# Kernel tuning notes

Measured on AMD Instinct MI355X. Metric: run time of the kernel, lower is better.

## Reference

```python
import jax, jax.numpy as jnp
import numpy as np

B, L, H, D = 64, 256, 16, 64   # batch, seq_len, heads, head_dim
C, K = 256, 8                  # wavelet c (== seq_len, required by attn@V), k
FACTOR = 5
SAMPLE_K = min(FACTOR * int(np.ceil(np.log(L))), C)  # U_part = 30
N_TOP = min(FACTOR * int(np.ceil(np.log(L))), C)     # u = 30
SCALE = 1.0 / float(np.sqrt(D))
ICH = L * D                    # Linear in-features: flattened (seq_len*D)
CK = C * K


def setup_inputs() -> dict:
    key = jax.random.key(0)
    ks = jax.random.split(key, 10)
    std = 1.0 / float(np.sqrt(ICH))
    def lin(kw, kb):
        return (jax.random.uniform(kw, (CK, ICH), jnp.float32, -std, std),
                jax.random.uniform(kb, (CK,), jnp.float32, -std, std))
    Wq_w, Wq_b = lin(ks[3], ks[4])
    Wk_w, Wk_b = lin(ks[5], ks[6])
    Wv_w, Wv_b = lin(ks[7], ks[8])
    return {
        "queries": jax.random.normal(ks[0], (B, L, H, D), jnp.float32),
        "keys":    jax.random.normal(ks[1], (B, L, H, D), jnp.float32),
        "values":  jax.random.normal(ks[2], (B, L, H, D), jnp.float32),
        "Wq_w": Wq_w, "Wq_b": Wq_b,
        "Wk_w": Wk_w, "Wk_b": Wk_b,
        "Wv_w": Wv_w, "Wv_b": Wv_b,
        "index_sample": jax.random.randint(ks[9], (C, SAMPLE_K), 0, C),
        "attn_mask": jnp.zeros((1,), bool),  # unused: module overwrites it with ProbMask
    }


def reference(queries, keys, values, Wq_w, Wq_b, Wk_w, Wk_b, Wv_w, Wv_b, index_sample, attn_mask):
    # [B,L,H,D] -> [B,H,L,D]
    q = jnp.swapaxes(queries, 1, 2)
    k = jnp.swapaxes(keys, 1, 2)
    v = jnp.swapaxes(values, 1, 2)

    def wavelet(x, W, b):
        # flatten (L,D) per head, project to c*k, reshape to [B,H,C,K]
        return (x.reshape(B, H, L * D) @ W.T + b).reshape(B, H, C, K)

    qw = wavelet(q, Wq_w, Wq_b)   # [B,H,C,K]
    kw = wavelet(k, Wk_w, Wk_b)   # [B,H,C,K]
    _vw = wavelet(v, Wv_w, Wv_b)  # computed then unused, as in the torch source

    # _prob_QK: sample SAMPLE_K keys per query position
    K_samp = kw[:, :, index_sample, :]                        # [B,H,C,S,K]
    QKs = jnp.einsum('bhck,bhcsk->bhcs', qw, K_samp)          # [B,H,C,S]
    M = QKs.max(-1) - QKs.sum(-1) / C                         # sparsity measure
    idx = jax.lax.top_k(M, N_TOP)[1]                          # [B,H,U] top queries
    Q_red = jnp.take_along_axis(qw, idx[..., None], axis=2)   # [B,H,U,K]
    scores = jnp.einsum('bhuk,bhck->bhuc', Q_red, kw) * SCALE # [B,H,U,C]

    # ProbMask: causal triu(1) rows gathered at idx
    tri = jnp.triu(jnp.ones((L, C), bool), 1)
    scores = jnp.where(tri[idx], -jnp.inf, scores)
    attn = jax.nn.softmax(scores, axis=-1)

    # initial context = cumsum of V (mask_flag=True); scatter updated rows
    ctx = jnp.cumsum(v, axis=2)                               # [B,H,L,D]
    upd = jnp.einsum('bhuc,bhcd->bhud', attn, v)              # C == L
    b_i = jnp.arange(B)[:, None, None]
    h_i = jnp.arange(H)[None, :, None]
    return ctx.at[b_i, h_i, idx].set(upd)                     # [B,H,L,D]
```

## Files before the change

### kernel.cpp

```cpp
#include <hip/hip_runtime.h>

#define NC 256
#define NK 8
#define NS 30
#define ICHN 16384
#define CKN 2048
#define MROWS 1024
#define PLANE ((size_t)MROWS * CKN)
#define SCLQ (1.0f / 65536.0f)

typedef _Float16 h4 __attribute__((ext_vector_type(4)));
typedef _Float16 h8 __attribute__((ext_vector_type(8)));
typedef float f4v __attribute__((ext_vector_type(4)));

__device__ __forceinline__ void split4(const float4& x, h4& hi, h4& lo) {
  const float* xp = &x.x;
#pragma unroll
  for (int j = 0; j < 4; ++j) {
    float xs = xp[j] * 256.0f;
    _Float16 hh = (_Float16)xs;
    hi[j] = hh;
    lo[j] = (_Float16)(xs - (float)hh);
  }
}

__global__ __launch_bounds__(512, 2) void gemm_split3(
    const float* __restrict__ qin, const float* __restrict__ kin,
    const float* __restrict__ Wq, const float* __restrict__ Wk,
    float* __restrict__ P, int KS, int KL, int nsteps) {
  __shared__ __align__(16) _Float16 ldsA[2][256][64];
  __shared__ __align__(16) _Float16 ldsB[2][256][64];

  const int tm = blockIdx.x & 3;
  const int tn = blockIdx.x >> 2;
  const int ksi = blockIdx.y;
  const int z = blockIdx.z;
  const float* act = z ? kin : qin;
  const float* W = z ? Wk : Wq;
  float* outp = P + (size_t)(z * KS + ksi) * PLANE;

  const int tid = threadIdx.x;
  const int r = tid >> 1;
  const int g = tid & 1;
  const int R = tm * 256 + r;
  const float* aP = act + (size_t)(R >> 4) * 262144 + (R & 15) * 64 +
                    (size_t)ksi * KL * 16 + g * 16;
  const int n = tn * 256 + r;
  const float* bP = W + (size_t)n * 16384 + (size_t)ksi * KL + g * 16;

  const int swW = r & 7;
  const int oh0 = r * 64 + (((4 * g + 0) ^ swW) << 3);
  const int ol0 = r * 64 + (((4 * g + 1) ^ swW) << 3);
  const int oh1 = r * 64 + (((4 * g + 2) ^ swW) << 3);
  const int ol1 = r * 64 + (((4 * g + 3) ^ swW) << 3);

  const int lane = tid & 63;
  const int wv = tid >> 6;
  const int wm = wv >> 2;
  const int wn = wv & 3;
  const int lr = lane & 15;
  const int lk = lane >> 4;
  const int swR = lr & 7;
  const int aOffH = (wm * 128 + lr) * 64 + (((2 * lk) ^ swR) << 3);
  const int aOffL = (wm * 128 + lr) * 64 + (((2 * lk + 1) ^ swR) << 3);
  const int bOffH = (wn * 64 + lr) * 64 + (((2 * lk) ^ swR) << 3);
  const int bOffL = (wn * 64 + lr) * 64 + (((2 * lk + 1) ^ swR) << 3);

  f4v acc[8][4];
#pragma unroll
  for (int i = 0; i < 8; ++i)
#pragma unroll
    for (int j = 0; j < 4; ++j) acc[i][j] = (f4v){0.f, 0.f, 0.f, 0.f};

  float4 aS[4], bS[4];

  auto LOADT = [&](int s) {
    const size_t aoff = (size_t)(s >> 1) * 1024 + (s & 1) * 32;
    const size_t boff = (size_t)s * 32;
#pragma unroll
    for (int c = 0; c < 4; ++c) {
      aS[c] = *(const float4*)(aP + aoff + c * 4);
      bS[c] = *(const float4*)(bP + boff + c * 4);
    }
  };
  auto WRITES = [&](int bufi) {
    _Float16* bA = &ldsA[bufi][0][0];
    _Float16* bB = &ldsB[bufi][0][0];
    h4 h0, l0, h1, l1;
    split4(aS[0], h0, l0);
    split4(aS[1], h1, l1);
    *(h8*)(bA + oh0) = (h8){h0[0], h0[1], h0[2], h0[3], h1[0], h1[1], h1[2], h1[3]};
    *(h8*)(bA + ol0) = (h8){l0[0], l0[1], l0[2], l0[3], l1[0], l1[1], l1[2], l1[3]};
    split4(aS[2], h0, l0);
    split4(aS[3], h1, l1);
    *(h8*)(bA + oh1) = (h8){h0[0], h0[1], h0[2], h0[3], h1[0], h1[1], h1[2], h1[3]};
    *(h8*)(bA + ol1) = (h8){l0[0], l0[1], l0[2], l0[3], l1[0], l1[1], l1[2], l1[3]};
    split4(bS[0], h0, l0);
    split4(bS[1], h1, l1);
    *(h8*)(bB + oh0) = (h8){h0[0], h0[1], h0[2], h0[3], h1[0], h1[1], h1[2], h1[3]};
    *(h8*)(bB + ol0) = (h8){l0[0], l0[1], l0[2], l0[3], l1[0], l1[1], l1[2], l1[3]};
    split4(bS[2], h0, l0);
    split4(bS[3], h1, l1);
    *(h8*)(bB + oh1) = (h8){h0[0], h0[1], h0[2], h0[3], h1[0], h1[1], h1[2], h1[3]};
    *(h8*)(bB + ol1) = (h8){l0[0], l0[1], l0[2], l0[3], l1[0], l1[1], l1[2], l1[3]};
  };
  auto COMPUTE = [&](int bufi) {
    const _Float16* bA = &ldsA[bufi][0][0];
    const _Float16* bB = &ldsB[bufi][0][0];
    h8 Bh[4], Bl[4];
#pragma unroll
    for (int fn = 0; fn < 4; ++fn) {
      Bh[fn] = *(const h8*)(bB + bOffH + fn * 1024);
      Bl[fn] = *(const h8*)(bB + bOffL + fn * 1024);
    }
#pragma unroll
    for (int half = 0; half < 2; ++half) {
      h8 Ah[4], Al[4];
#pragma unroll
      for (int fr = 0; fr < 4; ++fr) {
        Ah[fr] = *(const h8*)(bA + aOffH + (half * 4 + fr) * 1024);
        Al[fr] = *(const h8*)(bA + aOffL + (half * 4 + fr) * 1024);
      }
      __builtin_amdgcn_s_setprio(1);
#pragma unroll
      for (int fr = 0; fr < 4; ++fr)
#pragma unroll
        for (int fn = 0; fn < 4; ++fn) {
          f4v a = acc[half * 4 + fr][fn];
          a = __builtin_amdgcn_mfma_f32_16x16x32_f16(Ah[fr], Bh[fn], a, 0, 0, 0);
          a = __builtin_amdgcn_mfma_f32_16x16x32_f16(Ah[fr], Bl[fn], a, 0, 0, 0);
          a = __builtin_amdgcn_mfma_f32_16x16x32_f16(Al[fr], Bh[fn], a, 0, 0, 0);
          acc[half * 4 + fr][fn] = a;
        }
      __builtin_amdgcn_s_setprio(0);
    }
  };

  LOADT(0);
  WRITES(0);
  __syncthreads();
  int cur = 0;
  for (int s = 0; s < nsteps; ++s) {
    if (s + 1 < nsteps) LOADT(s + 1);
    COMPUTE(cur);
    if (s + 1 < nsteps) WRITES(cur ^ 1);
    __syncthreads();
    cur ^= 1;
  }

#pragma unroll
  for (int fr = 0; fr < 8; ++fr)
#pragma unroll
    for (int fn = 0; fn < 4; ++fn) {
      int ocol = tn * 256 + wn * 64 + fn * 16 + lr;
#pragma unroll
      for (int j = 0; j < 4; ++j) {
        int orow = tm * 256 + wm * 128 + fr * 16 + lk * 4 + j;
        outp[(size_t)orow * CKN + ocol] = acc[fr][fn][j];
      }
    }
}

__global__ __launch_bounds__(256, 2) void attn_tail(
    const float* __restrict__ P, const float* __restrict__ bq,
    const float* __restrict__ bk, const float* __restrict__ values,
    const int* __restrict__ isamp, float* __restrict__ out, int KS) {
  __shared__ float kT[8][256];
  __shared__ __align__(16) _Float16 vT[64][256];
  __shared__ __align__(16) _Float16 Pm[32][256];
  __shared__ float qsel[NS][8];
  __shared__ float MvC[256];
  __shared__ float csum4[4][64];
  __shared__ int idxl[NS];
  __shared__ int flagl[256];

  const int bh = blockIdx.x;
  const int b = bh >> 4, h = bh & 15;
  const int tid = threadIdx.x;
  const int w = tid >> 6, lane = tid & 63;
  const float* qpl = P;
  const float* kpl = P + (size_t)KS * PLANE;
  float* obase = out + (size_t)bh * 16384;

  float qq[8];
  {
    float ks8[8];
    size_t rowo = (size_t)bh * CKN + tid * 8;
#pragma unroll
    for (int k = 0; k < 8; ++k) ks8[k] = 0.0f;
    for (int p = 0; p < KS; ++p) {
      float4 a0 = *(const float4*)(kpl + p * PLANE + rowo);
      float4 a1 = *(const float4*)(kpl + p * PLANE + rowo + 4);
      ks8[0] += a0.x; ks8[1] += a0.y; ks8[2] += a0.z; ks8[3] += a0.w;
      ks8[4] += a1.x; ks8[5] += a1.y; ks8[6] += a1.z; ks8[7] += a1.w;
    }
    float4 b0 = *(const float4*)(bk + tid * 8);
    float4 b1 = *(const float4*)(bk + tid * 8 + 4);
    const float* bp = &b0.x;
    kT[0][tid] = ks8[0] * SCLQ + b0.x; kT[1][tid] = ks8[1] * SCLQ + b0.y;
    kT[2][tid] = ks8[2] * SCLQ + b0.z; kT[3][tid] = ks8[3] * SCLQ + b0.w;
    kT[4][tid] = ks8[4] * SCLQ + b1.x; kT[5][tid] = ks8[5] * SCLQ + b1.y;
    kT[6][tid] = ks8[6] * SCLQ + b1.z; kT[7][tid] = ks8[7] * SCLQ + b1.w;
    (void)bp;
#pragma unroll
    for (int k = 0; k < 8; ++k) qq[k] = 0.0f;
    for (int p = 0; p < KS; ++p) {
      float4 a0 = *(const float4*)(qpl + p * PLANE + rowo);
      float4 a1 = *(const float4*)(qpl + p * PLANE + rowo + 4);
      qq[0] += a0.x; qq[1] += a0.y; qq[2] += a0.z; qq[3] += a0.w;
      qq[4] += a1.x; qq[5] += a1.y; qq[6] += a1.z; qq[7] += a1.w;
    }
    float4 c0 = *(const float4*)(bq + tid * 8);
    float4 c1 = *(const float4*)(bq + tid * 8 + 4);
    qq[0] = qq[0] * SCLQ + c0.x; qq[1] = qq[1] * SCLQ + c0.y;
    qq[2] = qq[2] * SCLQ + c0.z; qq[3] = qq[3] * SCLQ + c0.w;
    qq[4] = qq[4] * SCLQ + c1.x; qq[5] = qq[5] * SCLQ + c1.y;
    qq[6] = qq[6] * SCLQ + c1.z; qq[7] = qq[7] * SCLQ + c1.w;
    const float* vbase = values + (size_t)b * 262144 + h * 64;
#pragma unroll
    for (int rep = 0; rep < 16; ++rep) {
      int i = rep * 256 + tid;
      int c = i >> 4, dg = i & 15;
      float4 v = *(const float4*)(vbase + (size_t)c * 1024 + dg * 4);
      const float* vp = &v.x;
#pragma unroll
      for (int j = 0; j < 4; ++j) {
        int d = dg * 4 + j;
        vT[d][(((c >> 3) ^ (d & 7)) << 3) | (c & 7)] = (_Float16)vp[j];
      }
    }
    flagl[tid] = 0;
    if (tid < 64) {
#pragma unroll
      for (int rr = 30; rr < 32; ++rr) {
        int ci = tid >> 1;
        *(h4*)&Pm[rr][((ci ^ (rr & 7)) << 3) | ((tid * 4) & 7)] =
            (h4){(_Float16)0, (_Float16)0, (_Float16)0, (_Float16)0};
      }
    }
  }
  __syncthreads();

  {
    float mx = -INFINITY, sm = 0.0f;
    const int* ip = isamp + tid * NS;
#pragma unroll 6
    for (int s = 0; s < NS; ++s) {
      int j = ip[s];
      float dot = 0.0f;
#pragma unroll
      for (int k = 0; k < NK; ++k) dot += qq[k] * kT[k][j];
      mx = fmaxf(mx, dot);
      sm += dot;
    }
    MvC[tid] = mx - sm * (1.0f / 256.0f);
  }
  __syncthreads();

  if (tid < 64) {
    float m0 = MvC[tid], m1 = MvC[tid + 64], m2 = MvC[tid + 128], m3 = MvC[tid + 192];
    for (int u = 0; u < NS; ++u) {
      float bv = m0; int bi = tid;
      if (m1 > bv) { bv = m1; bi = tid + 64; }
      if (m2 > bv) { bv = m2; bi = tid + 128; }
      if (m3 > bv) { bv = m3; bi = tid + 192; }
#pragma unroll
      for (int off = 32; off > 0; off >>= 1) {
        float ov = __shfl_xor(bv, off);
        int oi = __shfl_xor(bi, off);
        if (ov > bv || (ov == bv && oi < bi)) { bv = ov; bi = oi; }
      }
      if (tid == 0) { idxl[u] = bi; flagl[bi] = u + 1; }
      if (tid == (bi & 63)) {
        switch (bi >> 6) {
          case 0: m0 = -INFINITY; break;
          case 1: m1 = -INFINITY; break;
          case 2: m2 = -INFINITY; break;
          default: m3 = -INFINITY; break;
        }
      }
    }
  }
  __syncthreads();

  if (tid < NS * 8) {
    int u = tid >> 3, k = tid & 7;
    size_t off = (size_t)bh * CKN + idxl[u] * 8 + k;
    float s = 0.0f;
    for (int p = 0; p < KS; ++p) s += qpl[p * PLANE + off];
    qsel[u][k] = s * SCLQ + bq[idxl[u] * 8 + k];
  }
  __syncthreads();

  for (int ui = w; ui < NS; ui += 4) {
    const int qi = idxl[ui];
    float qv[8];
#pragma unroll
    for (int k = 0; k < 8; ++k) qv[k] = qsel[ui][k];
    float sj[4];
#pragma unroll
    for (int j = 0; j < 4; ++j) {
      int c = j * 64 + lane;
      float s = 0.0f;
#pragma unroll
      for (int k = 0; k < NK; ++k) s += qv[k] * kT[k][c];
      sj[j] = (c > qi) ? -INFINITY : s * 0.125f;
    }
    float m = fmaxf(fmaxf(sj[0], sj[1]), fmaxf(sj[2], sj[3]));
#pragma unroll
    for (int off = 32; off > 0; off >>= 1) m = fmaxf(m, __shfl_xor(m, off));
    float pj[4], ts = 0.0f;
#pragma unroll
    for (int j = 0; j < 4; ++j) { pj[j] = __expf(sj[j] - m); ts += pj[j]; }
#pragma unroll
    for (int off = 32; off > 0; off >>= 1) ts += __shfl_xor(ts, off);
    float rinv = 1.0f / ts;
#pragma unroll
    for (int j = 0; j < 4; ++j) {
      int c = j * 64 + lane;
      Pm[ui][(((c >> 3) ^ (ui & 7)) << 3) | (c & 7)] = (_Float16)(pj[j] * rinv);
    }
  }
  __syncthreads();

  {
    const int lr = lane & 15, lk = lane >> 4;
    f4v pacc[2];
    pacc[0] = (f4v){0.f, 0.f, 0.f, 0.f};
    pacc[1] = (f4v){0.f, 0.f, 0.f, 0.f};
#pragma unroll
    for (int kc = 0; kc < 8; ++kc) {
      int cidx = kc * 4 + lk;
      h8 Bv = *(const h8*)&vT[w * 16 + lr][((cidx ^ (lr & 7)) << 3)];
#pragma unroll
      for (int mf = 0; mf < 2; ++mf) {
        h8 Ap = *(const h8*)&Pm[mf * 16 + lr][((cidx ^ (lr & 7)) << 3)];
        pacc[mf] = __builtin_amdgcn_mfma_f32_16x16x32_f16(Ap, Bv, pacc[mf], 0, 0, 0);
      }
    }
#pragma unroll
    for (int mf = 0; mf < 2; ++mf)
#pragma unroll
      for (int j = 0; j < 4; ++j) {
        int u = mf * 16 + lk * 4 + j;
        if (u < NS) obase[(size_t)idxl[u] * 64 + w * 16 + lr] = pacc[mf][j];
      }
  }

  {
    float cs = 0.0f;
#pragma unroll 8
    for (int i = 0; i < 64; ++i) {
      int c = w * 64 + i;
      cs += (float)vT[lane][(((c >> 3) ^ (lane & 7)) << 3) | (c & 7)];
    }
    csum4[w][lane] = cs;
    __syncthreads();
    float run = 0.0f;
    for (int j2 = 0; j2 < w; ++j2) run += csum4[j2][lane];
    for (int i = 0; i < 64; ++i) {
      int l = w * 64 + i;
      run += (float)vT[lane][(((l >> 3) ^ (lane & 7)) << 3) | (l & 7)];
      if (!flagl[l]) obase[(size_t)l * 64 + lane] = run;
    }
  }
}

extern "C" void kernel_launch(void* const* d_in, const int* in_sizes, int n_in,
                              void* d_out, int out_size, void* d_ws, size_t ws_size,
                              hipStream_t stream) {
  (void)in_sizes; (void)n_in; (void)out_size;
  const float* queries = (const float*)d_in[0];
  const float* keys = (const float*)d_in[1];
  const float* values = (const float*)d_in[2];
  const float* Wq_w = (const float*)d_in[3];
  const float* Wq_b = (const float*)d_in[4];
  const float* Wk_w = (const float*)d_in[5];
  const float* Wk_b = (const float*)d_in[6];
  const int* index_sample = (const int*)d_in[9];
  float* out = (float*)d_out;

  float* P = (float*)d_ws;

  const int KS = (ws_size >= (size_t)8 * PLANE * 4) ? 4 : 2;
  const int KL = ICHN / KS;
  const int nsteps = KL / 32;

  dim3 gridG(32, KS, 2);
  gemm_split3<<<gridG, 512, 0, stream>>>(queries, keys, Wq_w, Wk_w, P, KS, KL, nsteps);
  attn_tail<<<dim3(MROWS), 256, 0, stream>>>(P, Wq_b, Wk_b, values, index_sample, out, KS);
}
```

Baseline: 454.9 us.

## Interleave global prefetch, LDS reads and split MFMA phases; remap block order

The GEMM main loop is split into three MFMA phases, with fragment reads from shared memory and the global prefetch loads for A and B spread between them and separated by extra barriers, so memory latency hides behind matrix instructions. The grid becomes 1D with the row tile as the slowest index, so blocks that share the same activation rows run at nearby times and reuse the activation data in cache. This adds two more block-wide barriers per k-step and keeps more fragments live in registers at once, which could lower occupancy or cause spills.

```diff
diff --git a/kernel.cpp b/kernel.cpp
--- a/kernel.cpp
+++ b/kernel.cpp
@@ -27,32 +27,34 @@
 __global__ __launch_bounds__(512, 2) void gemm_split3(
     const float* __restrict__ qin, const float* __restrict__ kin,
     const float* __restrict__ Wq, const float* __restrict__ Wk,
-    float* __restrict__ P, int KS, int KL, int nsteps) {
+    float* __restrict__ P, int KS, int KL, int nsteps, int groups) {
   __shared__ __align__(16) _Float16 ldsA[2][256][64];
   __shared__ __align__(16) _Float16 ldsB[2][256][64];
 
-  const int tm = blockIdx.x & 3;
-  const int tn = blockIdx.x >> 2;
-  const int ksi = blockIdx.y;
-  const int z = blockIdx.z;
+  const int bx = blockIdx.x;
+  const int tm = bx / groups;
+  const int g = bx - tm * groups;
+  const int tn = g & 7;
+  const int ksi = (g >> 3) % KS;
+  const int z = g / (8 * KS);
   const float* act = z ? kin : qin;
   const float* W = z ? Wk : Wq;
   float* outp = P + (size_t)(z * KS + ksi) * PLANE;
 
   const int tid = threadIdx.x;
   const int r = tid >> 1;
-  const int g = tid & 1;
+  const int gg = tid & 1;
   const int R = tm * 256 + r;
   const float* aP = act + (size_t)(R >> 4) * 262144 + (R & 15) * 64 +
-                    (size_t)ksi * KL * 16 + g * 16;
+                    (size_t)ksi * KL * 16 + gg * 16;
   const int n = tn * 256 + r;
-  const float* bP = W + (size_t)n * 16384 + (size_t)ksi * KL + g * 16;
+  const float* bP = W + (size_t)n * 16384 + (size_t)ksi * KL + gg * 16;
 
   const int swW = r & 7;
-  const int oh0 = r * 64 + (((4 * g + 0) ^ swW) << 3);
-  const int ol0 = r * 64 + (((4 * g + 1) ^ swW) << 3);
-  const int oh1 = r * 64 + (((4 * g + 2) ^ swW) << 3);
-  const int ol1 = r * 64 + (((4 * g + 3) ^ swW) << 3);
+  const int oh0 = r * 64 + (((4 * gg + 0) ^ swW) << 3);
+  const int ol0 = r * 64 + (((4 * gg + 1) ^ swW) << 3);
+  const int oh1 = r * 64 + (((4 * gg + 2) ^ swW) << 3);
+  const int ol1 = r * 64 + (((4 * gg + 3) ^ swW) << 3);
 
   const int lane = tid & 63;
   const int wv = tid >> 6;
@@ -73,15 +75,17 @@
     for (int j = 0; j < 4; ++j) acc[i][j] = (f4v){0.f, 0.f, 0.f, 0.f};
 
   float4 aS[4], bS[4];
-
-  auto LOADT = [&](int s) {
+  h8 Bh[4], Bl[4], A0h[4], A0l[4], A1h[4], A1l[4];
+
+  auto LOADT_A = [&](int s) {
     const size_t aoff = (size_t)(s >> 1) * 1024 + (s & 1) * 32;
+#pragma unroll
+    for (int c = 0; c < 4; ++c) aS[c] = *(const float4*)(aP + aoff + c * 4);
+  };
+  auto LOADT_B = [&](int s) {
     const size_t boff = (size_t)s * 32;
 #pragma unroll
-    for (int c = 0; c < 4; ++c) {
-      aS[c] = *(const float4*)(aP + aoff + c * 4);
-      bS[c] = *(const float4*)(bP + boff + c * 4);
-    }
+    for (int c = 0; c < 4; ++c) bS[c] = *(const float4*)(bP + boff + c * 4);
   };
   auto WRITES = [&](int bufi) {
     _Float16* bA = &ldsA[bufi][0][0];
@@ -104,46 +108,87 @@
     *(h8*)(bB + oh1) = (h8){h0[0], h0[1], h0[2], h0[3], h1[0], h1[1], h1[2], h1[3]};
     *(h8*)(bB + ol1) = (h8){l0[0], l0[1], l0[2], l0[3], l1[0], l1[1], l1[2], l1[3]};
   };
-  auto COMPUTE = [&](int bufi) {
-    const _Float16* bA = &ldsA[bufi][0][0];
-    const _Float16* bB = &ldsB[bufi][0][0];
-    h8 Bh[4], Bl[4];
+
+  auto READ_B = [&](int bufi) {
+    const _Float16* b = &ldsB[bufi][0][0];
 #pragma unroll
     for (int fn = 0; fn < 4; ++fn) {
-      Bh[fn] = *(const h8*)(bB + bOffH + fn * 1024);
-      Bl[fn] = *(const h8*)(bB + bOffL + fn * 1024);
-    }
-#pragma unroll
-    for (int half = 0; half < 2; ++half) {
-      h8 Ah[4], Al[4];
-#pragma unroll
-      for (int fr = 0; fr < 4; ++fr) {
-        Ah[fr] = *(const h8*)(bA + aOffH + (half * 4 + fr) * 1024);
-        Al[fr] = *(const h8*)(bA + aOffL + (half * 4 + fr) * 1024);
-      }
-      __builtin_amdgcn_s_setprio(1);
-#pragma unroll
-      for (int fr = 0; fr < 4; ++fr)
-#pragma unroll
-        for (int fn = 0; fn < 4; ++fn) {
-          f4v a = acc[half * 4 + fr][fn];
-          a = __builtin_amdgcn_mfma_f32_16x16x32_f16(Ah[fr], Bh[fn], a, 0, 0, 0);
-          a = __builtin_amdgcn_mfma_f32_16x16x32_f16(Ah[fr], Bl[fn], a, 0, 0, 0);
-          a = __builtin_amdgcn_mfma_f32_16x16x32_f16(Al[fr], Bh[fn], a, 0, 0, 0);
-          acc[half * 4 + fr][fn] = a;
-        }
-      __builtin_amdgcn_s_setprio(0);
-    }
-  };
-
-  LOADT(0);
+      Bh[fn] = *(const h8*)(b + bOffH + fn * 1024);
+      Bl[fn] = *(const h8*)(b + bOffL + fn * 1024);
+    }
+  };
+  auto READ_A0 = [&](int bufi) {
+    const _Float16* a = &ldsA[bufi][0][0];
+#pragma unroll
+    for (int fr = 0; fr < 4; ++fr) {
+      A0h[fr] = *(const h8*)(a + aOffH + fr * 1024);
+      A0l[fr] = *(const h8*)(a + aOffL + fr * 1024);
+    }
+  };
+  auto READ_A1 = [&](int bufi) {
+    const _Float16* a = &ldsA[bufi][0][0];
+#pragma unroll
+    for (int fr = 0; fr < 4; ++fr) {
+      A1h[fr] = *(const h8*)(a + aOffH + (4 + fr) * 1024);
+      A1l[fr] = *(const h8*)(a + aOffL + (4 + fr) * 1024);
+    }
+  };
+  auto MFMA_A = [&]() {
+    __builtin_amdgcn_s_setprio(1);
+#pragma unroll
+    for (int fr = 0; fr < 4; ++fr)
+#pragma unroll
+      for (int fn = 0; fn < 4; ++fn) {
+        f4v a = acc[fr][fn];
+        a = __builtin_amdgcn_mfma_f32_16x16x32_f16(A0h[fr], Bh[fn], a, 0, 0, 0);
+        a = __builtin_amdgcn_mfma_f32_16x16x32_f16(A0h[fr], Bl[fn], a, 0, 0, 0);
+        acc[fr][fn] = a;
+      }
+    __builtin_amdgcn_s_setprio(0);
+  };
+  auto MFMA_B = [&]() {
+    __builtin_amdgcn_s_setprio(1);
+#pragma unroll
+    for (int fr = 0; fr < 4; ++fr)
+#pragma unroll
+      for (int fn = 0; fn < 4; ++fn) {
+        acc[fr][fn] = __builtin_amdgcn_mfma_f32_16x16x32_f16(A0l[fr], Bh[fn], acc[fr][fn], 0, 0, 0);
+        acc[4 + fr][fn] = __builtin_amdgcn_mfma_f32_16x16x32_f16(A1h[fr], Bh[fn], acc[4 + fr][fn], 0, 0, 0);
+      }
+    __builtin_amdgcn_s_setprio(0);
+  };
+  auto MFMA_C = [&]() {
+    __builtin_amdgcn_s_setprio(1);
+#pragma unroll
+    for (int fr = 0; fr < 4; ++fr)
+#pragma unroll
+      for (int fn = 0; fn < 4; ++fn) {
+        f4v a = acc[4 + fr][fn];
+        a = __builtin_amdgcn_mfma_f32_16x16x32_f16(A1h[fr], Bl[fn], a, 0, 0, 0);
+        a = __builtin_amdgcn_mfma_f32_16x16x32_f16(A1l[fr], Bh[fn], a, 0, 0, 0);
+        acc[4 + fr][fn] = a;
+      }
+    __builtin_amdgcn_s_setprio(0);
+  };
+
+  LOADT_A(0);
+  LOADT_B(0);
   WRITES(0);
   __syncthreads();
   int cur = 0;
   for (int s = 0; s < nsteps; ++s) {
-    if (s + 1 < nsteps) LOADT(s + 1);
-    COMPUTE(cur);
-    if (s + 1 < nsteps) WRITES(cur ^ 1);
+    const bool pf = (s + 1 < nsteps);
+    READ_B(cur);
+    READ_A0(cur);
+    if (pf) LOADT_A(s + 1);
+    __syncthreads();
+    MFMA_A();
+    READ_A1(cur);
+    if (pf) LOADT_B(s + 1);
+    __syncthreads();
+    MFMA_B();
+    if (pf) WRITES(cur ^ 1);
+    MFMA_C();
     __syncthreads();
     cur ^= 1;
   }
@@ -196,12 +241,10 @@
     }
     float4 b0 = *(const float4*)(bk + tid * 8);
     float4 b1 = *(const float4*)(bk + tid * 8 + 4);
-    const float* bp = &b0.x;
     kT[0][tid] = ks8[0] * SCLQ + b0.x; kT[1][tid] = ks8[1] * SCLQ + b0.y;
     kT[2][tid] = ks8[2] * SCLQ + b0.z; kT[3][tid] = ks8[3] * SCLQ + b0.w;
     kT[4][tid] = ks8[4] * SCLQ + b1.x; kT[5][tid] = ks8[5] * SCLQ + b1.y;
     kT[6][tid] = ks8[6] * SCLQ + b1.z; kT[7][tid] = ks8[7] * SCLQ + b1.w;
-    (void)bp;
 #pragma unroll
     for (int k = 0; k < 8; ++k) qq[k] = 0.0f;
     for (int p = 0; p < KS; ++p) {
@@ -385,8 +428,9 @@
   const int KS = (ws_size >= (size_t)8 * PLANE * 4) ? 4 : 2;
   const int KL = ICHN / KS;
   const int nsteps = KL / 32;
-
-  dim3 gridG(32, KS, 2);
-  gemm_split3<<<gridG, 512, 0, stream>>>(queries, keys, Wq_w, Wk_w, P, KS, KL, nsteps);
+  const int groups = 8 * KS * 2;
+
+  gemm_split3<<<dim3(4 * groups), 512, 0, stream>>>(
+      queries, keys, Wq_w, Wk_w, P, KS, KL, nsteps, groups);
   attn_tail<<<dim3(MROWS), 256, 0, stream>>>(P, Wq_b, Wk_b, values, index_sample, out, KS);
 }
```

Measured after the change: 487.5 us. +7.2%, slower.

## Interleave global loads and LDS writes into four MFMA phases with explicit barriers

Applied to the files above, without the earlier changes.

Restructures the split-fp16 GEMM main loop into four phases of two fragment rows each. Global loads and LDS stores for the next tile are spread across the phases (A load, B load, A write, B write), separated by raw s_barrier and an lgkmcnt wait, instead of loading all at once and writing after the whole compute. The aim is to overlap memory traffic with MFMA work and smooth register and issue pressure. The cost is more barriers per step, and the raw barriers without an lgkmcnt wait before every phase carry some ordering risk.

```diff
diff --git a/kernel.cpp b/kernel.cpp
--- a/kernel.cpp
+++ b/kernel.cpp
@@ -13,6 +13,9 @@
 typedef _Float16 h8 __attribute__((ext_vector_type(8)));
 typedef float f4v __attribute__((ext_vector_type(4)));
 
+#define BAR() __builtin_amdgcn_s_barrier()
+#define FENCE_LGKM() asm volatile("s_waitcnt lgkmcnt(0)" ::: "memory")
+
 __device__ __forceinline__ void split4(const float4& x, h4& hi, h4& lo) {
   const float* xp = &x.x;
 #pragma unroll
@@ -41,18 +44,18 @@
 
   const int tid = threadIdx.x;
   const int r = tid >> 1;
-  const int g = tid & 1;
+  const int gg = tid & 1;
   const int R = tm * 256 + r;
   const float* aP = act + (size_t)(R >> 4) * 262144 + (R & 15) * 64 +
-                    (size_t)ksi * KL * 16 + g * 16;
+                    (size_t)ksi * KL * 16 + gg * 16;
   const int n = tn * 256 + r;
-  const float* bP = W + (size_t)n * 16384 + (size_t)ksi * KL + g * 16;
+  const float* bP = W + (size_t)n * 16384 + (size_t)ksi * KL + gg * 16;
 
   const int swW = r & 7;
-  const int oh0 = r * 64 + (((4 * g + 0) ^ swW) << 3);
-  const int ol0 = r * 64 + (((4 * g + 1) ^ swW) << 3);
-  const int oh1 = r * 64 + (((4 * g + 2) ^ swW) << 3);
-  const int ol1 = r * 64 + (((4 * g + 3) ^ swW) << 3);
+  const int oh0 = r * 64 + (((4 * gg + 0) ^ swW) << 3);
+  const int ol0 = r * 64 + (((4 * gg + 1) ^ swW) << 3);
+  const int oh1 = r * 64 + (((4 * gg + 2) ^ swW) << 3);
+  const int ol1 = r * 64 + (((4 * gg + 3) ^ swW) << 3);
 
   const int lane = tid & 63;
   const int wv = tid >> 6;
@@ -73,19 +76,20 @@
     for (int j = 0; j < 4; ++j) acc[i][j] = (f4v){0.f, 0.f, 0.f, 0.f};
 
   float4 aS[4], bS[4];
-
-  auto LOADT = [&](int s) {
+  h8 Bh[4], Bl[4];
+
+  auto LOADT_A = [&](int s) {
     const size_t aoff = (size_t)(s >> 1) * 1024 + (s & 1) * 32;
+#pragma unroll
+    for (int c = 0; c < 4; ++c) aS[c] = *(const float4*)(aP + aoff + c * 4);
+  };
+  auto LOADT_B = [&](int s) {
     const size_t boff = (size_t)s * 32;
 #pragma unroll
-    for (int c = 0; c < 4; ++c) {
-      aS[c] = *(const float4*)(aP + aoff + c * 4);
-      bS[c] = *(const float4*)(bP + boff + c * 4);
-    }
+    for (int c = 0; c < 4; ++c) bS[c] = *(const float4*)(bP + boff + c * 4);
   };
-  auto WRITES = [&](int bufi) {
+  auto WRITES_A = [&](int bufi) {
     _Float16* bA = &ldsA[bufi][0][0];
-    _Float16* bB = &ldsB[bufi][0][0];
     h4 h0, l0, h1, l1;
     split4(aS[0], h0, l0);
     split4(aS[1], h1, l1);
@@ -95,6 +99,10 @@
     split4(aS[3], h1, l1);
     *(h8*)(bA + oh1) = (h8){h0[0], h0[1], h0[2], h0[3], h1[0], h1[1], h1[2], h1[3]};
     *(h8*)(bA + ol1) = (h8){l0[0], l0[1], l0[2], l0[3], l1[0], l1[1], l1[2], l1[3]};
+  };
+  auto WRITES_B = [&](int bufi) {
+    _Float16* bB = &ldsB[bufi][0][0];
+    h4 h0, l0, h1, l1;
     split4(bS[0], h0, l0);
     split4(bS[1], h1, l1);
     *(h8*)(bB + oh0) = (h8){h0[0], h0[1], h0[2], h0[3], h1[0], h1[1], h1[2], h1[3]};
@@ -104,47 +112,118 @@
     *(h8*)(bB + oh1) = (h8){h0[0], h0[1], h0[2], h0[3], h1[0], h1[1], h1[2], h1[3]};
     *(h8*)(bB + ol1) = (h8){l0[0], l0[1], l0[2], l0[3], l1[0], l1[1], l1[2], l1[3]};
   };
-  auto COMPUTE = [&](int bufi) {
-    const _Float16* bA = &ldsA[bufi][0][0];
-    const _Float16* bB = &ldsB[bufi][0][0];
-    h8 Bh[4], Bl[4];
-#pragma unroll
-    for (int fn = 0; fn < 4; ++fn) {
-      Bh[fn] = *(const h8*)(bB + bOffH + fn * 1024);
-      Bl[fn] = *(const h8*)(bB + bOffL + fn * 1024);
-    }
-#pragma unroll
-    for (int half = 0; half < 2; ++half) {
-      h8 Ah[4], Al[4];
-#pragma unroll
-      for (int fr = 0; fr < 4; ++fr) {
-        Ah[fr] = *(const h8*)(bA + aOffH + (half * 4 + fr) * 1024);
-        Al[fr] = *(const h8*)(bA + aOffL + (half * 4 + fr) * 1024);
-      }
-      __builtin_amdgcn_s_setprio(1);
-#pragma unroll
-      for (int fr = 0; fr < 4; ++fr)
-#pragma unroll
-        for (int fn = 0; fn < 4; ++fn) {
-          f4v a = acc[half * 4 + fr][fn];
-          a = __builtin_amdgcn_mfma_f32_16x16x32_f16(Ah[fr], Bh[fn], a, 0, 0, 0);
-          a = __builtin_amdgcn_mfma_f32_16x16x32_f16(Ah[fr], Bl[fn], a, 0, 0, 0);
-          a = __builtin_amdgcn_mfma_f32_16x16x32_f16(Al[fr], Bh[fn], a, 0, 0, 0);
-          acc[half * 4 + fr][fn] = a;
-        }
-      __builtin_amdgcn_s_setprio(0);
-    }
-  };
-
-  LOADT(0);
-  WRITES(0);
-  __syncthreads();
+
+  LOADT_A(0);
+  LOADT_B(0);
+  WRITES_A(0);
+  WRITES_B(0);
+  FENCE_LGKM();
+  BAR();
+
   int cur = 0;
   for (int s = 0; s < nsteps; ++s) {
-    if (s + 1 < nsteps) LOADT(s + 1);
-    COMPUTE(cur);
-    if (s + 1 < nsteps) WRITES(cur ^ 1);
-    __syncthreads();
+    const bool pf = (s + 1 < nsteps);
+    const _Float16* bA = &ldsA[cur][0][0];
+    const _Float16* bB = &ldsB[cur][0][0];
+
+    {
+#pragma unroll
+      for (int fn = 0; fn < 4; ++fn) {
+        Bh[fn] = *(const h8*)(bB + bOffH + fn * 1024);
+        Bl[fn] = *(const h8*)(bB + bOffL + fn * 1024);
+      }
+      h8 Ah0 = *(const h8*)(bA + aOffH + 0 * 1024);
+      h8 Al0 = *(const h8*)(bA + aOffL + 0 * 1024);
+      h8 Ah1 = *(const h8*)(bA + aOffH + 1 * 1024);
+      h8 Al1 = *(const h8*)(bA + aOffL + 1 * 1024);
+      if (pf) LOADT_A(s + 1);
+      BAR();
+      __builtin_amdgcn_s_setprio(1);
+#pragma unroll
+      for (int fn = 0; fn < 4; ++fn) {
+        f4v a0 = acc[0][fn], a1 = acc[1][fn];
+        a0 = __builtin_amdgcn_mfma_f32_16x16x32_f16(Ah0, Bh[fn], a0, 0, 0, 0);
+        a1 = __builtin_amdgcn_mfma_f32_16x16x32_f16(Ah1, Bh[fn], a1, 0, 0, 0);
+        a0 = __builtin_amdgcn_mfma_f32_16x16x32_f16(Ah0, Bl[fn], a0, 0, 0, 0);
+        a1 = __builtin_amdgcn_mfma_f32_16x16x32_f16(Ah1, Bl[fn], a1, 0, 0, 0);
+        a0 = __builtin_amdgcn_mfma_f32_16x16x32_f16(Al0, Bh[fn], a0, 0, 0, 0);
+        a1 = __builtin_amdgcn_mfma_f32_16x16x32_f16(Al1, Bh[fn], a1, 0, 0, 0);
+        acc[0][fn] = a0; acc[1][fn] = a1;
+      }
+      __builtin_amdgcn_s_setprio(0);
+      BAR();
+    }
+
+    {
+      h8 Ah0 = *(const h8*)(bA + aOffH + 2 * 1024);
+      h8 Al0 = *(const h8*)(bA + aOffL + 2 * 1024);
+      h8 Ah1 = *(const h8*)(bA + aOffH + 3 * 1024);
+      h8 Al1 = *(const h8*)(bA + aOffL + 3 * 1024);
+      if (pf) LOADT_B(s + 1);
+      BAR();
+      __builtin_amdgcn_s_setprio(1);
+#pragma unroll
+      for (int fn = 0; fn < 4; ++fn) {
+        f4v a0 = acc[2][fn], a1 = acc[3][fn];
+        a0 = __builtin_amdgcn_mfma_f32_16x16x32_f16(Ah0, Bh[fn], a0, 0, 0, 0);
+        a1 = __builtin_amdgcn_mfma_f32_16x16x32_f16(Ah1, Bh[fn], a1, 0, 0, 0);
+        a0 = __builtin_amdgcn_mfma_f32_16x16x32_f16(Ah0, Bl[fn], a0, 0, 0, 0);
+        a1 = __builtin_amdgcn_mfma_f32_16x16x32_f16(Ah1, Bl[fn], a1, 0, 0, 0);
+        a0 = __builtin_amdgcn_mfma_f32_16x16x32_f16(Al0, Bh[fn], a0, 0, 0, 0);
+        a1 = __builtin_amdgcn_mfma_f32_16x16x32_f16(Al1, Bh[fn], a1, 0, 0, 0);
+        acc[2][fn] = a0; acc[3][fn] = a1;
+      }
+      __builtin_amdgcn_s_setprio(0);
+      BAR();
+    }
+
+    {
+      h8 Ah0 = *(const h8*)(bA + aOffH + 4 * 1024);
+      h8 Al0 = *(const h8*)(bA + aOffL + 4 * 1024);
+      h8 Ah1 = *(const h8*)(bA + aOffH + 5 * 1024);
+      h8 Al1 = *(const h8*)(bA + aOffL + 5 * 1024);
+      if (pf) WRITES_A(cur ^ 1);
+      BAR();
+      __builtin_amdgcn_s_setprio(1);
+#pragma unroll
+      for (int fn = 0; fn < 4; ++fn) {
+        f4v a0 = acc[4][fn], a1 = acc[5][fn];
+        a0 = __builtin_amdgcn_mfma_f32_16x16x32_f16(Ah0, Bh[fn], a0, 0, 0, 0);
+        a1 = __builtin_amdgcn_mfma_f32_16x16x32_f16(Ah1, Bh[fn], a1, 0, 0, 0);
+        a0 = __builtin_amdgcn_mfma_f32_16x16x32_f16(Ah0, Bl[fn], a0, 0, 0, 0);
+        a1 = __builtin_amdgcn_mfma_f32_16x16x32_f16(Ah1, Bl[fn], a1, 0, 0, 0);
+        a0 = __builtin_amdgcn_mfma_f32_16x16x32_f16(Al0, Bh[fn], a0, 0, 0, 0);
+        a1 = __builtin_amdgcn_mfma_f32_16x16x32_f16(Al1, Bh[fn], a1, 0, 0, 0);
+        acc[4][fn] = a0; acc[5][fn] = a1;
+      }
+      __builtin_amdgcn_s_setprio(0);
+      BAR();
+    }
+
+    {
+      h8 Ah0 = *(const h8*)(bA + aOffH + 6 * 1024);
+      h8 Al0 = *(const h8*)(bA + aOffL + 6 * 1024);
+      h8 Ah1 = *(const h8*)(bA + aOffH + 7 * 1024);
+      h8 Al1 = *(const h8*)(bA + aOffL + 7 * 1024);
+      if (pf) WRITES_B(cur ^ 1);
+      FENCE_LGKM();
+      BAR();
+      __builtin_amdgcn_s_setprio(1);
+#pragma unroll
+      for (int fn = 0; fn < 4; ++fn) {
+        f4v a0 = acc[6][fn], a1 = acc[7][fn];
+        a0 = __builtin_amdgcn_mfma_f32_16x16x32_f16(Ah0, Bh[fn], a0, 0, 0, 0);
+        a1 = __builtin_amdgcn_mfma_f32_16x16x32_f16(Ah1, Bh[fn], a1, 0, 0, 0);
+        a0 = __builtin_amdgcn_mfma_f32_16x16x32_f16(Ah0, Bl[fn], a0, 0, 0, 0);
+        a1 = __builtin_amdgcn_mfma_f32_16x16x32_f16(Ah1, Bl[fn], a1, 0, 0, 0);
+        a0 = __builtin_amdgcn_mfma_f32_16x16x32_f16(Al0, Bh[fn], a0, 0, 0, 0);
+        a1 = __builtin_amdgcn_mfma_f32_16x16x32_f16(Al1, Bh[fn], a1, 0, 0, 0);
+        acc[6][fn] = a0; acc[7][fn] = a1;
+      }
+      __builtin_amdgcn_s_setprio(0);
+      BAR();
+    }
+
     cur ^= 1;
   }
 
@@ -196,12 +275,10 @@
     }
     float4 b0 = *(const float4*)(bk + tid * 8);
     float4 b1 = *(const float4*)(bk + tid * 8 + 4);
-    const float* bp = &b0.x;
     kT[0][tid] = ks8[0] * SCLQ + b0.x; kT[1][tid] = ks8[1] * SCLQ + b0.y;
     kT[2][tid] = ks8[2] * SCLQ + b0.z; kT[3][tid] = ks8[3] * SCLQ + b0.w;
     kT[4][tid] = ks8[4] * SCLQ + b1.x; kT[5][tid] = ks8[5] * SCLQ + b1.y;
     kT[6][tid] = ks8[6] * SCLQ + b1.z; kT[7][tid] = ks8[7] * SCLQ + b1.w;
-    (void)bp;
 #pragma unroll
     for (int k = 0; k < 8; ++k) qq[k] = 0.0f;
     for (int p = 0; p < KS; ++p) {
```

Result: slower. 533.1 us (+17.2%).
